# Kernel optimization log

Hardware: AMD Instinct MI355X
Metric: run time of the kernel (lower is better)

## Reference

```python
import jax, jax.numpy as jnp
import numpy as np

PAIR_KEY_BASE = 20000  # token_max + 1
POS_WEIGHT = 1.0
NEG_WEIGHT = 1.0
EPS = 1e-8


def _isin_sorted(x, sorted_keys):
    # torch.isin equivalent given a sorted 1-D key set
    idx = jnp.searchsorted(sorted_keys, x)
    idx = jnp.clip(idx, 0, sorted_keys.shape[0] - 1)
    return sorted_keys[idx] == x


def setup_inputs() -> dict:
    key = jax.random.key(0)
    k_ids, k_tf, k_act, k_prior, k_u, k_v = jax.random.split(key, 6)
    B, S, D, M = 8, 2048, 64, 200000
    input_ids = jax.random.randint(k_ids, (B, S), 0, PAIR_KEY_BASE, dtype=jnp.int32)
    tf_mask = jax.random.randint(k_tf, (B, S), 0, 2) == 1
    active_gene_mask = jax.random.randint(k_act, (B, S), 0, 2) == 1
    # prior GRN pair keys: src*base + tgt, sorted (duplicates are harmless for isin)
    prior_pair_keys = jnp.sort(jax.random.randint(
        k_prior, (M,), 0, PAIR_KEY_BASE * PAIR_KEY_BASE, dtype=jnp.int32))
    # u, v small positive so u @ v^T lands mostly inside (0, 1) before clamping
    u = jax.random.uniform(k_u, (B, S, D), dtype=jnp.float32) * 0.1
    v = jax.random.uniform(k_v, (B, S, D), dtype=jnp.float32) * 0.1
    return {"input_ids": input_ids, "tf_mask": tf_mask,
            "active_gene_mask": active_gene_mask,
            "prior_pair_keys": prior_pair_keys, "u": u, "v": v}


def reference(input_ids, tf_mask, active_gene_mask, prior_pair_keys, u, v):
    # supervise: TF rows x active-gene cols  [B,S,S]
    supervise = tf_mask[:, :, None] & active_gene_mask[:, None, :]
    # pair keys for every (src, tgt) position pair  [B,S,S]
    pair_keys = input_ids[:, :, None] * PAIR_KEY_BASE + input_ids[:, None, :]
    positive = _isin_sorted(pair_keys, prior_pair_keys) & supervise
    target = positive.astype(jnp.float32)
    # edge probabilities, clamped like torch: [B,S,S]
    edge_prob = jnp.clip(jnp.einsum('bsd,btd->bst', u, v), EPS, 1.0 - EPS)
    # binary cross entropy, reduction='none'
    loss = -(target * jnp.log(edge_prob) + (1.0 - target) * jnp.log1p(-edge_prob))
    weight = target * POS_WEIGHT + (1.0 - target) * NEG_WEIGHT
    # neg_sample_ratio=None -> sampled_mask == supervise_mask
    m = supervise.astype(jnp.float32)
    numer = jnp.sum(loss * weight * m)
    denom = jnp.sum(weight * m)
    return numer / (denom + EPS)
```

## Files before the change

### kernel.cpp

```cpp
#include <hip/hip_runtime.h>
#include <math.h>

#define BB 8
#define SS 2048
#define DD 64
#define PAIR_BASE 20000
#define CEPS 1e-8f
#define NROWS (BB * SS)
#define MAIN_BLOCKS (16 * 16 * BB)
#define PPMAX 1024
#define PREP_BLOCKS (128 + BB + BB + 1)
#define POISON_WORD 0xAAAAAAAAu
#define CANARY_DONE 0x5A5A5A5Au

typedef __bf16 bf16x8 __attribute__((ext_vector_type(8)));
typedef __bf16 bf16x4 __attribute__((ext_vector_type(4)));
typedef float  f32x4  __attribute__((ext_vector_type(4)));

struct Ws {
    int byteMode;
    unsigned int canary;
    int mc[BB];
    int nc[BB];
    float mpart[MAIN_BLOCKS];
    float ppart[PPMAX];
    int cheadR[BB * PAIR_BASE];
    int cnextR[NROWS];
    int cheadC[BB * PAIR_BASE];
    int cnextC[NROWS];
    __bf16 Uc[(size_t)BB * SS * DD];
    __bf16 Vc[(size_t)BB * SS * DD];
};

__device__ __forceinline__ bool read_mask(const void* p, int i, int byteMode) {
    if (byteMode) return ((const unsigned char*)p)[i] != 0;
    return ((const int*)p)[i] != 0;
}

__device__ __forceinline__ int detect_bm(const void* tf_raw, int tid, int* badl) {
    if (tid == 0) *badl = 0;
    __syncthreads();
    if (((const unsigned int*)tf_raw)[tid] > 1u) atomicOr(badl, 1);
    __syncthreads();
    return *badl;
}

__global__ __launch_bounds__(1024) void prep_kernel(
    const int* __restrict__ ids,
    const void* __restrict__ tf_raw,
    const void* __restrict__ act_raw,
    const float* __restrict__ u,
    const float* __restrict__ v,
    Ws* __restrict__ ws)
{
    __shared__ int badl;
    __shared__ int wsum[16], wbase[16], stot;
    __shared__ unsigned short cidx[SS];

    const int blk  = blockIdx.x;
    const int tid  = threadIdx.x;
    const int w    = tid >> 6;
    const int lane = tid & 63;

    if (blk < 128) {
        const int phase = blk >> 6;
        const int b     = (blk >> 3) & 7;
        const int slice = blk & 7;
        const int bm = detect_bm(tf_raw, tid, &badl);
        const unsigned long long below = ((unsigned long long)1 << lane) - 1;

        const void* mraw = phase ? act_raw : tf_raw;
        const int e0 = b * SS + 2 * tid;
        const int m0 = read_mask(mraw, e0,     bm) ? 1 : 0;
        const int m1 = read_mask(mraw, e0 + 1, bm) ? 1 : 0;
        const unsigned long long k0 = __ballot(m0 != 0);
        const unsigned long long k1 = __ballot(m1 != 0);
        const int exclw = __popcll(k0 & below) + __popcll(k1 & below);
        if (lane == 0) wsum[w] = __popcll(k0) + __popcll(k1);
        __syncthreads();
        if (tid == 0) {
            int run = 0;
            #pragma unroll
            for (int k = 0; k < 16; ++k) { wbase[k] = run; run += wsum[k]; }
            stot = run;
        }
        __syncthreads();
        const int excl = wbase[w] + exclw;
        if (m0) cidx[excl]      = (unsigned short)(2 * tid);
        if (m1) cidx[excl + m0] = (unsigned short)(2 * tid + 1);
        __syncthreads();
        const int total = stot;
        if (tid == 0 && slice == 0) {
            if (phase) ws->nc[b] = total; else ws->mc[b] = total;
        }
        const int tpad = (total + 127) & ~127;
        const int rbeg = slice * 256;
        const int rend = min(rbeg + 256, tpad);
        __bf16* dst = (phase ? ws->Vc : ws->Uc) + (size_t)b * SS * DD;
        const float* src = (phase ? v : u) + (size_t)b * SS * DD;
        const int r_off = tid >> 4, c = tid & 15;
        #pragma unroll
        for (int p4 = 0; p4 < 4; ++p4) {
            const int r = rbeg + p4 * 64 + r_off;
            if (r < rend) {
                bf16x4 hv;
                if (r < total) {
                    const float4 f = *(const float4*)(src + (size_t)cidx[r] * DD + c * 4);
                    hv = (bf16x4){ (__bf16)f.x, (__bf16)f.y, (__bf16)f.z, (__bf16)f.w };
                } else {
                    hv = (bf16x4){ (__bf16)0.f, (__bf16)0.f, (__bf16)0.f, (__bf16)0.f };
                }
                *(bf16x4*)(dst + (size_t)r * DD + c * 4) = hv;
            }
        }
    } else if (blk < 128 + BB) {
        const int b = blk - 128;
        const bool poisoned = (ws->canary == POISON_WORD);
        const int bm = detect_bm(tf_raw, tid, &badl);
        int* head = ws->cheadR + b * PAIR_BASE;
        if (!poisoned) {
            for (int i = tid; i < PAIR_BASE; i += 1024) head[i] = -1;
            __syncthreads();
        }
        for (int s = tid; s < SS; s += 1024) {
            if (read_mask(tf_raw, b * SS + s, bm)) {
                const int id = ids[b * SS + s];
                const int old = atomicExch(&head[id], s);
                ws->cnextR[b * SS + s] = old;
            }
        }
    } else if (blk < 128 + 2 * BB) {
        const int b = blk - (128 + BB);
        const bool poisoned = (ws->canary == POISON_WORD);
        const int bm = detect_bm(tf_raw, tid, &badl);
        int* head = ws->cheadC + b * PAIR_BASE;
        if (!poisoned) {
            for (int i = tid; i < PAIR_BASE; i += 1024) head[i] = -1;
            __syncthreads();
        }
        for (int t = tid; t < SS; t += 1024) {
            if (read_mask(act_raw, b * SS + t, bm)) {
                const int id = ids[b * SS + t];
                const int old = atomicExch(&head[id], t);
                ws->cnextC[b * SS + t] = old;
            }
        }
    } else {
        const int bm = detect_bm(tf_raw, tid, &badl);
        if (tid == 0) ws->byteMode = bm;
    }
}

__global__ __launch_bounds__(256) void work_kernel(
    const int* __restrict__ prior, int M, int npos,
    const float* __restrict__ u,
    const float* __restrict__ v,
    Ws* __restrict__ ws)
{
    __shared__ __align__(16) __bf16 Ulds[128 * 72];
    __shared__ __align__(16) __bf16 Vlds[128 * 72];
    __shared__ float wsumS[4];

    const int bid  = blockIdx.x;
    const int tid  = threadIdx.x;
    const int w    = tid >> 6;
    const int lane = tid & 63;

    float lsum = 0.f;
    float* slot;

    if (bid < npos) {
        const int i = bid * 256 + tid;
        slot = &ws->ppart[bid];

        if (i < M) {
            const int key = prior[i];
            const bool dup = (i > 0) && (prior[i - 1] == key);
            if (!dup) {
                const unsigned int uk  = (unsigned int)key;
                const unsigned int src = uk / PAIR_BASE;
                const unsigned int tgt = uk - src * PAIR_BASE;
                int rh[BB];
                #pragma unroll
                for (int b = 0; b < BB; ++b)
                    rh[b] = ws->cheadR[b * PAIR_BASE + (int)src];
                int th[BB];
                #pragma unroll
                for (int b = 0; b < BB; ++b)
                    th[b] = (rh[b] >= 0) ? ws->cheadC[b * PAIR_BASE + (int)tgt] : -1;
                #pragma unroll
                for (int b = 0; b < BB; ++b) {
                    if (th[b] < 0) continue;
                    const int* nxtR = ws->cnextR + b * SS;
                    const int* nxtC = ws->cnextC + b * SS;
                    for (int r = rh[b]; r >= 0; r = nxtR[r]) {
                        const float* urow = u + (size_t)(b * SS + r) * DD;
                        for (int t = th[b]; t >= 0; t = nxtC[t]) {
                            const float* vrow = v + (size_t)(b * SS + t) * DD;
                            float dot = 0.f;
                            #pragma unroll
                            for (int k2 = 0; k2 < DD; k2 += 4) {
                                float4 a = *(const float4*)(urow + k2);
                                float4 c = *(const float4*)(vrow + k2);
                                dot += (float)(__bf16)a.x * (float)(__bf16)c.x;
                                dot += (float)(__bf16)a.y * (float)(__bf16)c.y;
                                dot += (float)(__bf16)a.z * (float)(__bf16)c.z;
                                dot += (float)(__bf16)a.w * (float)(__bf16)c.w;
                            }
                            float p = fminf(fmaxf(dot, CEPS), 1.0f - CEPS);
                            float q = fminf(fmaxf(1.0f - dot, CEPS), 1.0f - CEPS);
                            lsum += __logf(q) - __logf(p);
                        }
                    }
                }
            }
        }
    } else {
        const int gid = bid - npos;
        const int b  = gid >> 8;
        const int by = (gid >> 4) & 15;
        const int bx = gid & 15;
        const int s0 = by * 128;
        const int t0 = bx * 128;
        slot = &ws->mpart[gid];

        const int mcp = (ws->mc[b] + 127) & ~127;
        const int ncp = (ws->nc[b] + 127) & ~127;
        if (s0 < mcp && t0 < ncp) {
            const __bf16* ub = ws->Uc + (size_t)(b * SS + s0) * DD;
            const __bf16* vb = ws->Vc + (size_t)(b * SS + t0) * DD;
            #pragma unroll
            for (int it = 0; it < 4; ++it) {
                int li = tid + it * 256;
                int r  = li >> 3;
                int c8 = li & 7;
                *(bf16x8*)&Ulds[r * 72 + c8 * 8] = *(const bf16x8*)(ub + r * DD + c8 * 8);
                *(bf16x8*)&Vlds[r * 72 + c8 * 8] = *(const bf16x8*)(vb + r * DD + c8 * 8);
            }
            __syncthreads();

            const int quad = lane >> 4;
            const int l15  = lane & 15;
            const int wm0  = (w >> 1) * 64;
            const int wn0  = (w & 1) * 64;

            f32x4 acc[4][4];
            #pragma unroll
            for (int i = 0; i < 4; ++i)
                #pragma unroll
                for (int j = 0; j < 4; ++j)
                    acc[i][j] = (f32x4){0.f, 0.f, 0.f, 0.f};

            #pragma unroll
            for (int kh = 0; kh < 2; ++kh) {
                const int kcol = kh * 32 + quad * 8;
                bf16x8 af[4], bfr[4];
                #pragma unroll
                for (int ti = 0; ti < 4; ++ti)
                    af[ti] = *(const bf16x8*)&Ulds[(wm0 + ti * 16 + l15) * 72 + kcol];
                #pragma unroll
                for (int tj = 0; tj < 4; ++tj)
                    bfr[tj] = *(const bf16x8*)&Vlds[(wn0 + tj * 16 + l15) * 72 + kcol];
                #pragma unroll
                for (int ti = 0; ti < 4; ++ti)
                    #pragma unroll
                    for (int tj = 0; tj < 4; ++tj)
                        acc[ti][tj] = __builtin_amdgcn_mfma_f32_16x16x32_bf16(
                            af[ti], bfr[tj], acc[ti][tj], 0, 0, 0);
            }

            #pragma unroll
            for (int ti = 0; ti < 4; ++ti)
                #pragma unroll
                for (int r = 0; r < 4; ++r)
                    #pragma unroll
                    for (int tj = 0; tj < 4; ++tj) {
                        float q = 1.0f - acc[ti][tj][r];
                        q = fminf(fmaxf(q, CEPS), 1.0f - CEPS);
                        lsum += __logf(q);
                    }
            lsum = -lsum;
        }
    }

    #pragma unroll
    for (int o = 32; o > 0; o >>= 1)
        lsum += __shfl_down(lsum, o, 64);
    if (lane == 0) wsumS[w] = lsum;
    __syncthreads();
    if (tid == 0)
        *slot = wsumS[0] + wsumS[1] + wsumS[2] + wsumS[3];
}

__global__ __launch_bounds__(256) void finalize_kernel(Ws* __restrict__ ws,
                                                       int npp,
                                                       float* __restrict__ out) {
    __shared__ double sred[256];
    const int tid = threadIdx.x;
    double s = 0.0;
    for (int i = tid; i < MAIN_BLOCKS; i += 256) s += (double)ws->mpart[i];
    for (int i = tid; i < npp;         i += 256) s += (double)ws->ppart[i];
    sred[tid] = s;
    __syncthreads();
    for (int o = 128; o > 0; o >>= 1) {
        if (tid < o) sred[tid] += sred[tid + o];
        __syncthreads();
    }
    if (tid == 0) {
        double denom = 0.0;
        for (int b = 0; b < BB; ++b)
            denom += (double)ws->mc[b] * (double)ws->nc[b];
        out[0] = (float)(sred[0] / (denom + 1e-8));
        ws->canary = CANARY_DONE;
    }
}

extern "C" void kernel_launch(void* const* d_in, const int* in_sizes, int n_in,
                              void* d_out, int out_size, void* d_ws, size_t ws_size,
                              hipStream_t stream) {
    (void)n_in; (void)out_size; (void)ws_size;
    const int*   ids   = (const int*)d_in[0];
    const void*  tf    = d_in[1];
    const void*  act   = d_in[2];
    const int*   prior = (const int*)d_in[3];
    const int    M     = in_sizes[3];
    const float* u     = (const float*)d_in[4];
    const float* v     = (const float*)d_in[5];
    Ws* ws = (Ws*)d_ws;
    float* out = (float*)d_out;

    int npos = (M + 255) / 256;
    if (npos > PPMAX) npos = PPMAX;

    prep_kernel<<<PREP_BLOCKS, 1024, 0, stream>>>(ids, tf, act, u, v, ws);
    work_kernel<<<npos + MAIN_BLOCKS, 256, 0, stream>>>(prior, M, npos, u, v, ws);
    finalize_kernel<<<1, 256, 0, stream>>>(ws, npos, out);
}
```

Before: 103.8 us.

## Split fused work kernel into positives and GEMM kernels; double prep gather blocks

The combined kernel that held both the sparse positive-pair loop and the tiled MFMA GEMM blocks is split into two separate launches. The GEMM kernel no longer carries the divergent positive-path code, which may lower its register and LDS use. The prep gather phase also uses twice as many blocks, each converting 128 rows instead of 256, to spread the compaction and bf16 conversion more widely. The cost is an extra kernel launch, plus the positive and GEMM work now running one after the other instead of sharing one grid.

```diff
diff --git a/kernel.cpp b/kernel.cpp
--- a/kernel.cpp
+++ b/kernel.cpp
@@ -9,7 +9,7 @@
 #define NROWS (BB * SS)
 #define MAIN_BLOCKS (16 * 16 * BB)
 #define PPMAX 1024
-#define PREP_BLOCKS (128 + BB + BB + 1)
+#define PREP_BLOCKS (256 + BB + BB + 1)
 #define POISON_WORD 0xAAAAAAAAu
 #define CANARY_DONE 0x5A5A5A5Au
 
@@ -62,10 +62,10 @@
     const int w    = tid >> 6;
     const int lane = tid & 63;
 
-    if (blk < 128) {
-        const int phase = blk >> 6;
-        const int b     = (blk >> 3) & 7;
-        const int slice = blk & 7;
+    if (blk < 256) {
+        const int phase = blk >> 7;
+        const int b     = (blk >> 4) & 7;
+        const int slice = blk & 15;
         const int bm = detect_bm(tf_raw, tid, &badl);
         const unsigned long long below = ((unsigned long long)1 << lane) - 1;
 
@@ -94,13 +94,13 @@
             if (phase) ws->nc[b] = total; else ws->mc[b] = total;
         }
         const int tpad = (total + 127) & ~127;
-        const int rbeg = slice * 256;
-        const int rend = min(rbeg + 256, tpad);
+        const int rbeg = slice * 128;
+        const int rend = min(rbeg + 128, tpad);
         __bf16* dst = (phase ? ws->Vc : ws->Uc) + (size_t)b * SS * DD;
         const float* src = (phase ? v : u) + (size_t)b * SS * DD;
         const int r_off = tid >> 4, c = tid & 15;
         #pragma unroll
-        for (int p4 = 0; p4 < 4; ++p4) {
+        for (int p4 = 0; p4 < 2; ++p4) {
             const int r = rbeg + p4 * 64 + r_off;
             if (r < rend) {
                 bf16x4 hv;
@@ -113,8 +113,8 @@
                 *(bf16x4*)(dst + (size_t)r * DD + c * 4) = hv;
             }
         }
-    } else if (blk < 128 + BB) {
-        const int b = blk - 128;
+    } else if (blk < 256 + BB) {
+        const int b = blk - 256;
         const bool poisoned = (ws->canary == POISON_WORD);
         const int bm = detect_bm(tf_raw, tid, &badl);
         int* head = ws->cheadR + b * PAIR_BASE;
@@ -129,8 +129,8 @@
                 ws->cnextR[b * SS + s] = old;
             }
         }
-    } else if (blk < 128 + 2 * BB) {
-        const int b = blk - (128 + BB);
+    } else if (blk < 256 + 2 * BB) {
+        const int b = blk - (256 + BB);
         const bool poisoned = (ws->canary == POISON_WORD);
         const int bm = detect_bm(tf_raw, tid, &badl);
         int* head = ws->cheadC + b * PAIR_BASE;
@@ -151,137 +151,151 @@
     }
 }
 
-__global__ __launch_bounds__(256) void work_kernel(
-    const int* __restrict__ prior, int M, int npos,
+__global__ __launch_bounds__(256) void positives_kernel(
+    const int* __restrict__ prior, int M,
     const float* __restrict__ u,
     const float* __restrict__ v,
+    Ws* __restrict__ ws)
+{
+    __shared__ float wsumS[4];
+    const int bid  = blockIdx.x;
+    const int tid  = threadIdx.x;
+    const int w    = tid >> 6;
+    const int lane = tid & 63;
+
+    float lsum = 0.f;
+    const int i = bid * 256 + tid;
+    if (i < M) {
+        const int key = prior[i];
+        const bool dup = (i > 0) && (prior[i - 1] == key);
+        if (!dup) {
+            const unsigned int uk  = (unsigned int)key;
+            const unsigned int src = uk / PAIR_BASE;
+            const unsigned int tgt = uk - src * PAIR_BASE;
+            int rh[BB];
+            #pragma unroll
+            for (int b = 0; b < BB; ++b)
+                rh[b] = ws->cheadR[b * PAIR_BASE + (int)src];
+            int th[BB];
+            #pragma unroll
+            for (int b = 0; b < BB; ++b)
+                th[b] = (rh[b] >= 0) ? ws->cheadC[b * PAIR_BASE + (int)tgt] : -1;
+            #pragma unroll
+            for (int b = 0; b < BB; ++b) {
+                if (th[b] < 0) continue;
+                const int* nxtR = ws->cnextR + b * SS;
+                const int* nxtC = ws->cnextC + b * SS;
+                for (int r = rh[b]; r >= 0; r = nxtR[r]) {
+                    const float* urow = u + (size_t)(b * SS + r) * DD;
+                    for (int t = th[b]; t >= 0; t = nxtC[t]) {
+                        const float* vrow = v + (size_t)(b * SS + t) * DD;
+                        float dot = 0.f;
+                        #pragma unroll
+                        for (int k2 = 0; k2 < DD; k2 += 4) {
+                            float4 a = *(const float4*)(urow + k2);
+                            float4 c = *(const float4*)(vrow + k2);
+                            dot += (float)(__bf16)a.x * (float)(__bf16)c.x;
+                            dot += (float)(__bf16)a.y * (float)(__bf16)c.y;
+                            dot += (float)(__bf16)a.z * (float)(__bf16)c.z;
+                            dot += (float)(__bf16)a.w * (float)(__bf16)c.w;
+                        }
+                        float p = fminf(fmaxf(dot, CEPS), 1.0f - CEPS);
+                        float q = fminf(fmaxf(1.0f - dot, CEPS), 1.0f - CEPS);
+                        lsum += __logf(q) - __logf(p);
+                    }
+                }
+            }
+        }
+    }
+
+    #pragma unroll
+    for (int o = 32; o > 0; o >>= 1)
+        lsum += __shfl_down(lsum, o, 64);
+    if (lane == 0) wsumS[w] = lsum;
+    __syncthreads();
+    if (tid == 0)
+        ws->ppart[bid] = wsumS[0] + wsumS[1] + wsumS[2] + wsumS[3];
+}
+
+__global__ __launch_bounds__(256) void gemm_kernel(
     Ws* __restrict__ ws)
 {
     __shared__ __align__(16) __bf16 Ulds[128 * 72];
     __shared__ __align__(16) __bf16 Vlds[128 * 72];
     __shared__ float wsumS[4];
 
-    const int bid  = blockIdx.x;
+    const int gid  = blockIdx.x;
     const int tid  = threadIdx.x;
     const int w    = tid >> 6;
     const int lane = tid & 63;
 
+    const int b  = gid >> 8;
+    const int by = (gid >> 4) & 15;
+    const int bx = gid & 15;
+    const int s0 = by * 128;
+    const int t0 = bx * 128;
+
+    const int mcp = (ws->mc[b] + 127) & ~127;
+    const int ncp = (ws->nc[b] + 127) & ~127;
+    if (s0 >= mcp || t0 >= ncp) {
+        if (tid == 0) ws->mpart[gid] = 0.0f;
+        return;
+    }
+
+    const __bf16* ub = ws->Uc + (size_t)(b * SS + s0) * DD;
+    const __bf16* vb = ws->Vc + (size_t)(b * SS + t0) * DD;
+    #pragma unroll
+    for (int it = 0; it < 4; ++it) {
+        int li = tid + it * 256;
+        int r  = li >> 3;
+        int c8 = li & 7;
+        *(bf16x8*)&Ulds[r * 72 + c8 * 8] = *(const bf16x8*)(ub + r * DD + c8 * 8);
+        *(bf16x8*)&Vlds[r * 72 + c8 * 8] = *(const bf16x8*)(vb + r * DD + c8 * 8);
+    }
+    __syncthreads();
+
+    const int quad = lane >> 4;
+    const int l15  = lane & 15;
+    const int wm0  = (w >> 1) * 64;
+    const int wn0  = (w & 1) * 64;
+
+    f32x4 acc[4][4];
+    #pragma unroll
+    for (int i = 0; i < 4; ++i)
+        #pragma unroll
+        for (int j = 0; j < 4; ++j)
+            acc[i][j] = (f32x4){0.f, 0.f, 0.f, 0.f};
+
+    #pragma unroll
+    for (int kh = 0; kh < 2; ++kh) {
+        const int kcol = kh * 32 + quad * 8;
+        bf16x8 af[4], bfr[4];
+        #pragma unroll
+        for (int ti = 0; ti < 4; ++ti)
+            af[ti] = *(const bf16x8*)&Ulds[(wm0 + ti * 16 + l15) * 72 + kcol];
+        #pragma unroll
+        for (int tj = 0; tj < 4; ++tj)
+            bfr[tj] = *(const bf16x8*)&Vlds[(wn0 + tj * 16 + l15) * 72 + kcol];
+        #pragma unroll
+        for (int ti = 0; ti < 4; ++ti)
+            #pragma unroll
+            for (int tj = 0; tj < 4; ++tj)
+                acc[ti][tj] = __builtin_amdgcn_mfma_f32_16x16x32_bf16(
+                    af[ti], bfr[tj], acc[ti][tj], 0, 0, 0);
+    }
+
     float lsum = 0.f;
-    float* slot;
-
-    if (bid < npos) {
-        const int i = bid * 256 + tid;
-        slot = &ws->ppart[bid];
-
-        if (i < M) {
-            const int key = prior[i];
-            const bool dup = (i > 0) && (prior[i - 1] == key);
-            if (!dup) {
-                const unsigned int uk  = (unsigned int)key;
-                const unsigned int src = uk / PAIR_BASE;
-                const unsigned int tgt = uk - src * PAIR_BASE;
-                int rh[BB];
-                #pragma unroll
-                for (int b = 0; b < BB; ++b)
-                    rh[b] = ws->cheadR[b * PAIR_BASE + (int)src];
-                int th[BB];
-                #pragma unroll
-                for (int b = 0; b < BB; ++b)
-                    th[b] = (rh[b] >= 0) ? ws->cheadC[b * PAIR_BASE + (int)tgt] : -1;
-                #pragma unroll
-                for (int b = 0; b < BB; ++b) {
-                    if (th[b] < 0) continue;
-                    const int* nxtR = ws->cnextR + b * SS;
-                    const int* nxtC = ws->cnextC + b * SS;
-                    for (int r = rh[b]; r >= 0; r = nxtR[r]) {
-                        const float* urow = u + (size_t)(b * SS + r) * DD;
-                        for (int t = th[b]; t >= 0; t = nxtC[t]) {
-                            const float* vrow = v + (size_t)(b * SS + t) * DD;
-                            float dot = 0.f;
-                            #pragma unroll
-                            for (int k2 = 0; k2 < DD; k2 += 4) {
-                                float4 a = *(const float4*)(urow + k2);
-                                float4 c = *(const float4*)(vrow + k2);
-                                dot += (float)(__bf16)a.x * (float)(__bf16)c.x;
-                                dot += (float)(__bf16)a.y * (float)(__bf16)c.y;
-                                dot += (float)(__bf16)a.z * (float)(__bf16)c.z;
-                                dot += (float)(__bf16)a.w * (float)(__bf16)c.w;
-                            }
-                            float p = fminf(fmaxf(dot, CEPS), 1.0f - CEPS);
-                            float q = fminf(fmaxf(1.0f - dot, CEPS), 1.0f - CEPS);
-                            lsum += __logf(q) - __logf(p);
-                        }
-                    }
-                }
-            }
-        }
-    } else {
-        const int gid = bid - npos;
-        const int b  = gid >> 8;
-        const int by = (gid >> 4) & 15;
-        const int bx = gid & 15;
-        const int s0 = by * 128;
-        const int t0 = bx * 128;
-        slot = &ws->mpart[gid];
-
-        const int mcp = (ws->mc[b] + 127) & ~127;
-        const int ncp = (ws->nc[b] + 127) & ~127;
-        if (s0 < mcp && t0 < ncp) {
-            const __bf16* ub = ws->Uc + (size_t)(b * SS + s0) * DD;
-            const __bf16* vb = ws->Vc + (size_t)(b * SS + t0) * DD;
-            #pragma unroll
-            for (int it = 0; it < 4; ++it) {
-                int li = tid + it * 256;
-                int r  = li >> 3;
-                int c8 = li & 7;
-                *(bf16x8*)&Ulds[r * 72 + c8 * 8] = *(const bf16x8*)(ub + r * DD + c8 * 8);
-                *(bf16x8*)&Vlds[r * 72 + c8 * 8] = *(const bf16x8*)(vb + r * DD + c8 * 8);
-            }
-            __syncthreads();
-
-            const int quad = lane >> 4;
-            const int l15  = lane & 15;
-            const int wm0  = (w >> 1) * 64;
-            const int wn0  = (w & 1) * 64;
-
-            f32x4 acc[4][4];
-            #pragma unroll
-            for (int i = 0; i < 4; ++i)
-                #pragma unroll
-                for (int j = 0; j < 4; ++j)
-                    acc[i][j] = (f32x4){0.f, 0.f, 0.f, 0.f};
-
-            #pragma unroll
-            for (int kh = 0; kh < 2; ++kh) {
-                const int kcol = kh * 32 + quad * 8;
-                bf16x8 af[4], bfr[4];
-                #pragma unroll
-                for (int ti = 0; ti < 4; ++ti)
-                    af[ti] = *(const bf16x8*)&Ulds[(wm0 + ti * 16 + l15) * 72 + kcol];
-                #pragma unroll
-                for (int tj = 0; tj < 4; ++tj)
-                    bfr[tj] = *(const bf16x8*)&Vlds[(wn0 + tj * 16 + l15) * 72 + kcol];
-                #pragma unroll
-                for (int ti = 0; ti < 4; ++ti)
-                    #pragma unroll
-                    for (int tj = 0; tj < 4; ++tj)
-                        acc[ti][tj] = __builtin_amdgcn_mfma_f32_16x16x32_bf16(
-                            af[ti], bfr[tj], acc[ti][tj], 0, 0, 0);
-            }
-
-            #pragma unroll
-            for (int ti = 0; ti < 4; ++ti)
-                #pragma unroll
-                for (int r = 0; r < 4; ++r)
-                    #pragma unroll
-                    for (int tj = 0; tj < 4; ++tj) {
-                        float q = 1.0f - acc[ti][tj][r];
-                        q = fminf(fmaxf(q, CEPS), 1.0f - CEPS);
-                        lsum += __logf(q);
-                    }
-            lsum = -lsum;
-        }
-    }
+    #pragma unroll
+    for (int ti = 0; ti < 4; ++ti)
+        #pragma unroll
+        for (int r = 0; r < 4; ++r)
+            #pragma unroll
+            for (int tj = 0; tj < 4; ++tj) {
+                float q = 1.0f - acc[ti][tj][r];
+                q = fminf(fmaxf(q, CEPS), 1.0f - CEPS);
+                lsum += __logf(q);
+            }
+    lsum = -lsum;
 
     #pragma unroll
     for (int o = 32; o > 0; o >>= 1)
@@ -289,7 +303,7 @@
     if (lane == 0) wsumS[w] = lsum;
     __syncthreads();
     if (tid == 0)
-        *slot = wsumS[0] + wsumS[1] + wsumS[2] + wsumS[3];
+        ws->mpart[gid] = wsumS[0] + wsumS[1] + wsumS[2] + wsumS[3];
 }
 
 __global__ __launch_bounds__(256) void finalize_kernel(Ws* __restrict__ ws,
@@ -333,6 +347,8 @@
     if (npos > PPMAX) npos = PPMAX;
 
     prep_kernel<<<PREP_BLOCKS, 1024, 0, stream>>>(ids, tf, act, u, v, ws);
-    work_kernel<<<npos + MAIN_BLOCKS, 256, 0, stream>>>(prior, M, npos, u, v, ws);
+    if (npos > 0)
+        positives_kernel<<<npos, 256, 0, stream>>>(prior, M, u, v, ws);
+    gemm_kernel<<<MAIN_BLOCKS, 256, 0, stream>>>(ws);
     finalize_kernel<<<1, 256, 0, stream>>>(ws, npos, out);
 }
```

Result: slower. 106.4 us (+2.5%).
